# Optimization experiments

Measured on AMD Instinct MI355X. Metric: run time of the kernel, lower is better.

Reference implementation:

```python
import jax, jax.numpy as jnp
import numpy as np

RES = 512
STEPS = 128
SIGMA = 0.01


def _sample_cubic(curves, t):
    # curves: [N,4,2], t: [S] in [0,1]. De Casteljau, matching the torch module.
    p0, p1, p2, p3 = curves[:, 0], curves[:, 1], curves[:, 2], curves[:, 3]  # each [N,2]

    def lerp(a, b):  # [N,2] -> [N,2,S]
        return a[:, :, None] + (b - a)[:, :, None] * t

    a01, a12, a23 = lerp(p0, p1), lerp(p1, p2), lerp(p2, p3)
    qa = a01 + t * (a12 - a01)   # quadratic over first 3 points
    qb = a12 + t * (a23 - a12)   # quadratic over last 3 points
    curve = qa + t * (qb - qa)   # cubic, [N,2,S]
    # torch.cat([...], dim=1) over curves of shape [2,S] -> [2, N*S]
    return jnp.moveaxis(curve, 0, 1).reshape(2, -1)


def setup_inputs() -> dict:
    key = jax.random.key(0)
    curves = jax.random.uniform(key, (8, 4, 2), dtype=jnp.float32)
    return {"curves": curves}


def reference(curves) -> jnp.ndarray:
    t = jnp.linspace(0.0, 1.0, STEPS)
    curve = _sample_cubic(curves, t)  # [2, T], T = N*STEPS
    x, y = curve[0], curve[1]
    grid = jnp.arange(RES, dtype=curve.dtype) / RES  # pixel coords / res
    inv = 1.0 / (2.0 * SIGMA * SIGMA)
    # exp(-(dx^2+dy^2)/2s^2) factors exactly: raster[a,b] = sum_s Ex[a,s]*Ey[b,s]
    Ex = jnp.exp(-(x[None, :] - grid[:, None]) ** 2 * inv)  # [RES, T]
    Ey = jnp.exp(-(y[None, :] - grid[:, None]) ** 2 * inv)  # [RES, T]
    raster = Ex @ Ey.T  # [RES, RES], raster[a,b]
    # torch returns transpose(raster, 0, 1)
    return raster.T
```

## Files before the change

kernel.cpp:

```cpp
#include <hip/hip_runtime.h>


constexpr int RES_ = 512;
constexpr int TILE = 16;
constexpr int NPTS = 1024;
constexpr int CH   = 32;
constexpr float RAD = 33.0f / 512.0f;
constexpr float SENTINEL = 1.0e3f;

__global__ __launch_bounds__(256)
void bezier_sparse16(const float* __restrict__ curves, float* __restrict__ out) {
    __shared__ float lx[NPTS + CH], ly[NPTS + CH];
    __shared__ int count;
    __shared__ __align__(16) float ex_s[CH][TILE];
    __shared__ __align__(16) float ey_s[CH][TILE];

    const int tid  = threadIdx.x;
    const int lane = tid & 63;
    const int ibase = blockIdx.x * TILE;
    const int jbase = blockIdx.y * TILE;

    if (tid == 0) count = 0;
    __syncthreads();

    const float xlo = (float)ibase * (1.0f/512.0f) - RAD;
    const float xhi = (float)(ibase + TILE - 1) * (1.0f/512.0f) + RAD;
    const float ylo = (float)jbase * (1.0f/512.0f) - RAD;
    const float yhi = (float)(jbase + TILE - 1) * (1.0f/512.0f) + RAD;

#pragma unroll
    for (int e = 0; e < NPTS / 256; ++e) {
        int p = e * 256 + tid;
        int c = p >> 7;
        float t = (float)(p & 127) * (1.0f / 127.0f);
        const float* cp = curves + c * 8;
        float p0x = cp[0], p0y = cp[1];
        float p1x = cp[2], p1y = cp[3];
        float p2x = cp[4], p2y = cp[5];
        float p3x = cp[6], p3y = cp[7];
        float a01x = p0x + (p1x - p0x) * t, a01y = p0y + (p1y - p0y) * t;
        float a12x = p1x + (p2x - p1x) * t, a12y = p1y + (p2y - p1y) * t;
        float a23x = p2x + (p3x - p2x) * t, a23y = p2y + (p3y - p2y) * t;
        float qax = a01x + (a12x - a01x) * t, qay = a01y + (a12y - a01y) * t;
        float qbx = a12x + (a23x - a12x) * t, qby = a12y + (a23y - a12y) * t;
        float X = qax + (qbx - qax) * t;
        float Y = qay + (qby - qay) * t;

        bool keep = (X > xlo && X < xhi && Y > ylo && Y < yhi);
        unsigned long long mask = __ballot(keep);
        if (mask) {
            int nsurv  = __popcll(mask);
            int prefix = __popcll(mask & ((1ull << lane) - 1ull));
            int leader = __ffsll((long long)mask) - 1;
            int base_i = 0;
            if (lane == leader)
                base_i = atomicAdd(&count, nsurv);
            base_i = __shfl(base_i, leader);
            if (keep) {
                lx[base_i + prefix] = X;
                ly[base_i + prefix] = Y;
            }
        }
    }
    __syncthreads();
    const int M = count;

    if (tid < CH) {
        lx[M + tid] = SENTINEL;
        ly[M + tid] = SENTINEL;
    }
    __syncthreads();

    const int it = tid & 15, jt = tid >> 4;
    float acc0 = 0.f, acc1 = 0.f;

    const int Mp = (M + CH - 1) & ~(CH - 1);
    for (int base = 0; base < Mp; base += CH) {
#pragma unroll
        for (int e = 0; e < (CH * TILE) / 256; ++e) {
            int idx = e * 256 + tid;
            int kk  = idx >> 4;
            int ii  = idx & 15;
            float xv = lx[base + kk], yv = ly[base + kk];
            float dx = xv - (float)(ibase + ii) * (1.0f / 512.0f);
            float dy = yv - (float)(jbase + ii) * (1.0f / 512.0f);
            ex_s[kk][ii] = __expf(dx * dx * -5000.0f);
            ey_s[kk][ii] = __expf(dy * dy * -5000.0f);
        }
        __syncthreads();

#pragma unroll
        for (int k = 0; k < CH; k += 2) {
            acc0 = fmaf(ey_s[k][jt],     ex_s[k][it],     acc0);
            acc1 = fmaf(ey_s[k + 1][jt], ex_s[k + 1][it], acc1);
        }
        __syncthreads();
    }

    out[(size_t)(jbase + jt) * RES_ + (ibase + it)] = acc0 + acc1;
}

extern "C" void kernel_launch(void* const* d_in, const int* in_sizes, int n_in,
                              void* d_out, int out_size, void* d_ws, size_t ws_size,
                              hipStream_t stream) {
    const float* curves = (const float*)d_in[0];
    float* out = (float*)d_out;

    dim3 grid(RES_ / TILE, RES_ / TILE);
    bezier_sparse16<<<grid, dim3(256), 0, stream>>>(curves, out);
}
```

Baseline: 56.61 us.

## Double-buffer exp tiles, transpose layout for float4 reads, cull curves by bbox

Stages the Gaussian factor tiles into two shared buffers, so the next chunk's exps are computed while the current chunk is accumulated. This drops one barrier per chunk. The tiles are transposed to [pixel][point] with padding, so the inner product reads float4 vectors into four accumulators. Curves whose control-point bounding box misses the tile are skipped before Bezier evaluation. The cost is more shared memory, and the double-buffer sync pattern has to stay correct. Since a Bezier curve lies inside the convex hull of its control points, the bbox test is exact.

```diff
diff --git a/kernel.cpp b/kernel.cpp
--- a/kernel.cpp
+++ b/kernel.cpp
@@ -5,6 +5,7 @@
 constexpr int TILE = 16;
 constexpr int NPTS = 1024;
 constexpr int CH   = 32;
+constexpr int CHP  = CH + 4;
 constexpr float RAD = 33.0f / 512.0f;
 constexpr float SENTINEL = 1.0e3f;
 
@@ -12,26 +13,36 @@
 void bezier_sparse16(const float* __restrict__ curves, float* __restrict__ out) {
     __shared__ float lx[NPTS + CH], ly[NPTS + CH];
     __shared__ int count;
-    __shared__ __align__(16) float ex_s[CH][TILE];
-    __shared__ __align__(16) float ey_s[CH][TILE];
+    __shared__ int ovl[8];
+    __shared__ __align__(16) float ex_s[2][TILE][CHP];
+    __shared__ __align__(16) float ey_s[2][TILE][CHP];
 
     const int tid  = threadIdx.x;
     const int lane = tid & 63;
     const int ibase = blockIdx.x * TILE;
     const int jbase = blockIdx.y * TILE;
 
-    if (tid == 0) count = 0;
-    __syncthreads();
-
     const float xlo = (float)ibase * (1.0f/512.0f) - RAD;
     const float xhi = (float)(ibase + TILE - 1) * (1.0f/512.0f) + RAD;
     const float ylo = (float)jbase * (1.0f/512.0f) - RAD;
     const float yhi = (float)(jbase + TILE - 1) * (1.0f/512.0f) + RAD;
 
+    if (tid == 0) count = 0;
+    if (tid < 8) {
+        const float* cp = curves + tid * 8;
+        float bx0 = fminf(fminf(cp[0], cp[2]), fminf(cp[4], cp[6]));
+        float bx1 = fmaxf(fmaxf(cp[0], cp[2]), fmaxf(cp[4], cp[6]));
+        float by0 = fminf(fminf(cp[1], cp[3]), fminf(cp[5], cp[7]));
+        float by1 = fmaxf(fmaxf(cp[1], cp[3]), fmaxf(cp[5], cp[7]));
+        ovl[tid] = (bx1 > xlo && bx0 < xhi && by1 > ylo && by0 < yhi);
+    }
+    __syncthreads();
+
 #pragma unroll
     for (int e = 0; e < NPTS / 256; ++e) {
         int p = e * 256 + tid;
         int c = p >> 7;
+        if (!ovl[c]) continue;
         float t = (float)(p & 127) * (1.0f / 127.0f);
         const float* cp = curves + c * 8;
         float p0x = cp[0], p0y = cp[1];
@@ -72,10 +83,11 @@
     __syncthreads();
 
     const int it = tid & 15, jt = tid >> 4;
-    float acc0 = 0.f, acc1 = 0.f;
+    float acc0 = 0.f, acc1 = 0.f, acc2 = 0.f, acc3 = 0.f;
 
-    const int Mp = (M + CH - 1) & ~(CH - 1);
-    for (int base = 0; base < Mp; base += CH) {
+    const int nch = (M + CH - 1) / CH;
+
+    auto stage = [&](int b, int base) {
 #pragma unroll
         for (int e = 0; e < (CH * TILE) / 256; ++e) {
             int idx = e * 256 + tid;
@@ -84,20 +96,30 @@
             float xv = lx[base + kk], yv = ly[base + kk];
             float dx = xv - (float)(ibase + ii) * (1.0f / 512.0f);
             float dy = yv - (float)(jbase + ii) * (1.0f / 512.0f);
-            ex_s[kk][ii] = __expf(dx * dx * -5000.0f);
-            ey_s[kk][ii] = __expf(dy * dy * -5000.0f);
+            ex_s[b][ii][kk] = __expf(dx * dx * -5000.0f);
+            ey_s[b][ii][kk] = __expf(dy * dy * -5000.0f);
         }
+    };
+
+    if (nch > 0) stage(0, 0);
+    for (int c = 0; c < nch; ++c) {
         __syncthreads();
-
+        if (c + 1 < nch) stage((c + 1) & 1, (c + 1) * CH);
+        const int b = c & 1;
+        const float4* ax4 = reinterpret_cast<const float4*>(&ex_s[b][it][0]);
+        const float4* ay4 = reinterpret_cast<const float4*>(&ey_s[b][jt][0]);
 #pragma unroll
-        for (int k = 0; k < CH; k += 2) {
-            acc0 = fmaf(ey_s[k][jt],     ex_s[k][it],     acc0);
-            acc1 = fmaf(ey_s[k + 1][jt], ex_s[k + 1][it], acc1);
+        for (int k4 = 0; k4 < CH / 4; k4 += 2) {
+            float4 ax = ax4[k4],     ay = ay4[k4];
+            float4 bx = ax4[k4 + 1], by = ay4[k4 + 1];
+            acc0 = fmaf(ax.x, ay.x, acc0); acc1 = fmaf(ax.y, ay.y, acc1);
+            acc2 = fmaf(ax.z, ay.z, acc2); acc3 = fmaf(ax.w, ay.w, acc3);
+            acc0 = fmaf(bx.x, by.x, acc0); acc1 = fmaf(bx.y, by.y, acc1);
+            acc2 = fmaf(bx.z, by.z, acc2); acc3 = fmaf(bx.w, by.w, acc3);
         }
-        __syncthreads();
     }
 
-    out[(size_t)(jbase + jt) * RES_ + (ibase + it)] = acc0 + acc1;
+    out[(size_t)(jbase + jt) * RES_ + (ibase + it)] = (acc0 + acc1) + (acc2 + acc3);
 }
 
 extern "C" void kernel_launch(void* const* d_in, const int* in_sizes, int n_in,
```

Result: no change. 57.04 us (+0.8%).
